# Kernel optimization log

Measured on AMD Instinct MI355X. Metric: run time of the kernel, lower is better.

## Reference

```python
import jax, jax.numpy as jnp
import numpy as np

B, N, P, E, H, D, F, L = 16, 500, 100, 128, 8, 16, 512, 6
CLIP = 10.0  # logit_clipping


def _heads(x, h):
    b, n, _ = x.shape
    return x.reshape(b, n, h, -1).transpose(0, 2, 1, 3)  # [b,h,n,d]


def _mha(q, k, v, mask3=None):
    d = q.shape[-1]
    s = jnp.einsum('bhnd,bhmd->bhnm', q, k) / jnp.sqrt(jnp.asarray(d, q.dtype))
    if mask3 is not None:
        s = s + mask3[:, None, :, :]
    w = jax.nn.softmax(s, axis=-1)
    o = jnp.einsum('bhnm,bhmd->bhnd', w, v)
    b, h, n, dd = o.shape
    return o.transpose(0, 2, 1, 3).reshape(b, n, h * dd)


def _ff(x, w1, b1, w2, b2):
    return jax.nn.relu(x @ w1 + b1) @ w2 + b2


def _forward(depot_xy, node_xy, node_demand, load, cur_dist, ninf_mask,
             emb_depot_w, emb_depot_b, emb_node_w, emb_node_b,
             enc_wq, enc_wk, enc_wv, enc_comb_w, enc_comb_b,
             enc_ff1_w, enc_ff1_b, enc_ff2_w, enc_ff2_b,
             dec_wq_last, dec_wk, dec_wv, dec_comb_w, dec_comb_b,
             dec_cap_w, dec_ff1_w, dec_ff1_b, dec_ff2_w, dec_ff2_b,
             current_node):
    # ---------------- encoder ----------------
    node_xy_demand = jnp.concatenate([node_xy, node_demand[:, :, None]], axis=2)  # [B,N,3]
    x = jnp.concatenate([depot_xy @ emb_depot_w + emb_depot_b,
                         node_xy_demand @ emb_node_w + emb_node_b], axis=1)  # [B,N+1,E]
    for i in range(L):
        q = _heads(x @ enc_wq[i], H)
        k = _heads(x @ enc_wk[i], H)
        v = _heads(x @ enc_wv[i], H)
        mh = _mha(q, k, v) @ enc_comb_w[i] + enc_comb_b[i]
        o1 = x + mh
        x = o1 + _ff(o1, enc_ff1_w[i], enc_ff1_b[i], enc_ff2_w[i], enc_ff2_b[i])
    encoded_nodes = x  # [B, N+1, E]
    # decoder kv cache (set_kv)
    k = _heads(encoded_nodes @ dec_wk, H)
    v = _heads(encoded_nodes @ dec_wv, H)
    # ---------------- one decode step ----------------
    encoded_last = jnp.take_along_axis(encoded_nodes, current_node[:, :, None], axis=1)  # [B,P,E]
    input_cat = jnp.concatenate([encoded_last, load[:, :, None]], axis=2)  # [B,P,E+1]
    q = _heads(input_cat @ dec_wq_last, H)
    mh = _mha(q, k, v, mask3=ninf_mask) @ dec_comb_w + dec_comb_b
    mh = mh + encoded_last + load[:, :, None] @ dec_cap_w
    q_ref = _ff(mh, dec_ff1_w, dec_ff1_b, dec_ff2_w, dec_ff2_b) + mh
    score = jnp.einsum('bpe,bne->bpn', q_ref, encoded_nodes) / jnp.sqrt(jnp.asarray(E, q_ref.dtype))
    # distance-based noise injection
    dmin = cur_dist.min(axis=-1, keepdims=True)
    dmax = cur_dist.max(axis=-1, keepdims=True)
    norm_dist = (cur_dist - dmin) / (dmax - dmin + 1e-6)
    problem_size = ninf_mask.shape[2]
    nm = 50.0 / problem_size
    base_noise = jax.random.normal(jax.random.key(42), cur_dist.shape, cur_dist.dtype) * 0.2 + 0.5
    score = score - (1.0 - nm) * jnp.log(norm_dist + 1e-6) + base_noise * nm
    score = CLIP * jnp.tanh(score) + ninf_mask
    return jax.nn.softmax(score, axis=2)  # [B,P,N+1]


def setup_inputs() -> dict:
    key = jax.random.key(0)
    ks = iter(jax.random.split(key, 40))
    def rn(shape, s=0.02):
        return s * jax.random.normal(next(ks), shape, jnp.float32)
    return dict(
        depot_xy=jax.random.uniform(next(ks), (B, 1, 2), jnp.float32),
        node_xy=jax.random.uniform(next(ks), (B, N, 2), jnp.float32),
        node_demand=jax.random.uniform(next(ks), (B, N), jnp.float32),
        load=jax.random.uniform(next(ks), (B, P), jnp.float32),
        cur_dist=jax.random.uniform(next(ks), (B, P, N + 1), jnp.float32),
        ninf_mask=jnp.zeros((B, P, N + 1), jnp.float32),
        current_node=jax.random.randint(next(ks), (B, P), 0, N + 1),
        emb_depot_w=rn((2, E)), emb_depot_b=rn((E,)),
        emb_node_w=rn((3, E)), emb_node_b=rn((E,)),
        enc_wq=rn((L, E, H * D)), enc_wk=rn((L, E, H * D)), enc_wv=rn((L, E, H * D)),
        enc_comb_w=rn((L, H * D, E)), enc_comb_b=rn((L, E)),
        enc_ff1_w=rn((L, E, F)), enc_ff1_b=rn((L, F)),
        enc_ff2_w=rn((L, F, E)), enc_ff2_b=rn((L, E)),
        dec_wq_last=rn((E + 1, H * D)), dec_wk=rn((E, H * D)), dec_wv=rn((E, H * D)),
        dec_comb_w=rn((H * D, E)), dec_comb_b=rn((E,)),
        dec_cap_w=rn((1, E)),
        dec_ff1_w=rn((E, F)), dec_ff1_b=rn((F,)),
        dec_ff2_w=rn((F, E)), dec_ff2_b=rn((E,)),
    )


def reference(depot_xy, node_xy, node_demand, load, cur_dist, ninf_mask, current_node,
              emb_depot_w, emb_depot_b, emb_node_w, emb_node_b,
              enc_wq, enc_wk, enc_wv, enc_comb_w, enc_comb_b,
              enc_ff1_w, enc_ff1_b, enc_ff2_w, enc_ff2_b,
              dec_wq_last, dec_wk, dec_wv, dec_comb_w, dec_comb_b,
              dec_cap_w, dec_ff1_w, dec_ff1_b, dec_ff2_w, dec_ff2_b):
    return _forward(depot_xy, node_xy, node_demand, load, cur_dist, ninf_mask,
                    emb_depot_w, emb_depot_b, emb_node_w, emb_node_b,
                    enc_wq, enc_wk, enc_wv, enc_comb_w, enc_comb_b,
                    enc_ff1_w, enc_ff1_b, enc_ff2_w, enc_ff2_b,
                    dec_wq_last, dec_wk, dec_wv, dec_comb_w, dec_comb_b,
                    dec_cap_w, dec_ff1_w, dec_ff1_b, dec_ff2_w, dec_ff2_b,
                    current_node)
```

## Files before the change

### kernel.cpp

```cpp
#include <hip/hip_runtime.h>
#include <math.h>

#define Bb 16
#define Nn 500
#define NT 501
#define Pp 100
#define Ee 128
#define Hh 8
#define Dd 16
#define Ff 512
#define Ll 6
#define Mtok (Bb*NT)
#define PR (Bb*Pp)
#define TJ 32
#define SPLIT 4
#define KSEG 126
#define DSPLIT 16
#define DSEG 32
#define ENCP (6*128*384)
#define DECP (128*256)
#define SNP 512

__global__ __launch_bounds__(256) void pack_k(
    const float* __restrict__ ewq, const float* __restrict__ ewk, const float* __restrict__ ewv,
    const float* __restrict__ dwk, const float* __restrict__ dwv,
    float* __restrict__ encP, float* __restrict__ decP)
{
  int i = blockIdx.x*256 + threadIdx.x;
  if (i < ENCP) {
    int l = i / (128*384); int rem = i - l*128*384; int k = rem / 384; int n = rem - k*384;
    float v;
    if (n < 128)      v = ewq[((size_t)l*128 + k)*128 + n];
    else if (n < 256) v = ewk[((size_t)l*128 + k)*128 + (n-128)];
    else              v = ewv[((size_t)l*128 + k)*128 + (n-256)];
    encP[i] = v;
  } else {
    int j = i - ENCP;
    if (j < DECP) {
      int k = j >> 8; int n = j & 255;
      decP[j] = (n < 128) ? dwk[k*128 + n] : dwv[k*128 + (n-128)];
    }
  }
}

__global__ __launch_bounds__(256) void embed_k(
    const float* __restrict__ depot_xy, const float* __restrict__ node_xy,
    const float* __restrict__ node_demand,
    const float* __restrict__ wD, const float* __restrict__ bD,
    const float* __restrict__ wN, const float* __restrict__ bN,
    float* __restrict__ x)
{
  int t = blockIdx.x*256 + threadIdx.x;
  if (t >= Mtok*Ee) return;
  int e   = t & (Ee-1);
  int tok = t >> 7;
  int b   = tok / NT;
  int n   = tok - b*NT;
  float v;
  if (n == 0) {
    v = depot_xy[b*2+0]*wD[0*Ee+e] + depot_xy[b*2+1]*wD[1*Ee+e] + bD[e];
  } else {
    int nn = n - 1;
    float c0 = node_xy[(b*Nn + nn)*2 + 0];
    float c1 = node_xy[(b*Nn + nn)*2 + 1];
    float c2 = node_demand[b*Nn + nn];
    v = c0*wN[0*Ee+e] + c1*wN[1*Ee+e] + c2*wN[2*Ee+e] + bN[e];
  }
  x[(size_t)tok*Ee + e] = v;
}

__global__ __launch_bounds__(256) void gemm_k(
    const float* __restrict__ A, const float* __restrict__ W,
    const float* __restrict__ bias, const float* __restrict__ res,
    float* __restrict__ C, int M, int N, int K, int relu)
{
  __shared__ __align__(16) float As[2][16][68];
  __shared__ __align__(16) float Bs[2][16][68];
  int tid = threadIdx.x;
  int tx = tid & 15, ty = tid >> 4;
  int m0 = blockIdx.x * 64, n0 = blockIdx.y * 64;
  float acc[4][4];
  #pragma unroll
  for (int i=0;i<4;i++)
    #pragma unroll
    for (int j=0;j<4;j++) acc[i][j] = 0.f;

  int ar = tid >> 2;
  int ak = (tid & 3) << 2;
  int br = tid >> 4;
  int bc = (tid & 15) << 2;

  const float* Ap = A + (size_t)(m0 + ar)*K + ak;
  const float* Wp = W + (size_t)br*N + n0 + bc;
  bool aok = (m0 + ar) < M;

  float4 av = aok ? *(const float4*)(Ap) : make_float4(0.f,0.f,0.f,0.f);
  float4 wv = *(const float4*)(Wp);

  int nk = K >> 4;
  for (int t = 0; t < nk; ++t) {
    int cur = t & 1;
    As[cur][ak+0][ar] = av.x; As[cur][ak+1][ar] = av.y;
    As[cur][ak+2][ar] = av.z; As[cur][ak+3][ar] = av.w;
    *(float4*)(&Bs[cur][br][bc]) = wv;
    __syncthreads();
    if (t+1 < nk) {
      av = aok ? *(const float4*)(Ap + (t+1)*16) : make_float4(0.f,0.f,0.f,0.f);
      wv = *(const float4*)(Wp + (size_t)(t+1)*16*N);
    }
    #pragma unroll
    for (int k=0;k<16;k++){
      float4 a4 = *(const float4*)(&As[cur][k][ty*4]);
      float4 b4 = *(const float4*)(&Bs[cur][k][tx*4]);
      float avv[4] = {a4.x,a4.y,a4.z,a4.w};
      float bvv[4] = {b4.x,b4.y,b4.z,b4.w};
      #pragma unroll
      for (int i=0;i<4;i++)
        #pragma unroll
        for (int j=0;j<4;j++)
          acc[i][j] = fmaf(avv[i], bvv[j], acc[i][j]);
    }
  }

  float4 bv = make_float4(0.f,0.f,0.f,0.f);
  if (bias) bv = *(const float4*)(bias + n0 + tx*4);
  #pragma unroll
  for (int i=0;i<4;i++){
    int row = m0 + ty*4 + i;
    if (row >= M) continue;
    float4 o;
    o.x = acc[i][0] + bv.x; o.y = acc[i][1] + bv.y;
    o.z = acc[i][2] + bv.z; o.w = acc[i][3] + bv.w;
    if (relu){ o.x=fmaxf(o.x,0.f); o.y=fmaxf(o.y,0.f); o.z=fmaxf(o.z,0.f); o.w=fmaxf(o.w,0.f); }
    if (res){
      float4 rv = *(const float4*)(res + (size_t)row*N + n0 + tx*4);
      o.x += rv.x; o.y += rv.y; o.z += rv.z; o.w += rv.w;
    }
    *(float4*)(C + (size_t)row*N + n0 + tx*4) = o;
  }
}

__device__ __forceinline__ float dot4(float4 a, float4 b){
  return fmaf(a.x,b.x, fmaf(a.y,b.y, fmaf(a.z,b.z, a.w*b.w)));
}

__global__ __launch_bounds__(256, 1) void attn_enc_k(
    const float* __restrict__ QKV, float* __restrict__ part_o,
    float* __restrict__ part_l)
{
  int blk = blockIdx.x;
  int s  = blk % SPLIT;
  int bh = blk / SPLIT;
  int h  = bh & (Hh-1);
  int b  = bh >> 3;
  int tid = threadIdx.x;
  int p0 = tid;
  int p1 = tid + 256;
  const int klo = s*KSEG;
  int kseg = NT - klo; if (kseg > KSEG) kseg = KSEG;

  __shared__ __align__(16) float4 Ks[2][TJ][4];
  __shared__ __align__(16) float4 Vs[2][TJ][4];

  int row = (tid >> 2) & 31;
  int lc  = tid & 3;
  bool isV = tid >= 128;
  const int kvoff = isV ? 256 : 128;

  bool vbq = p1 < NT;

  const float4* qp0 = (const float4*)(QKV + ((size_t)(b*NT + p0))*384 + h*Dd);
  float4 qa0=qp0[0], qa1=qp0[1], qa2=qp0[2], qa3=qp0[3];
  float4 qb0,qb1,qb2,qb3;
  if (vbq) {
    const float4* qp1 = (const float4*)(QKV + ((size_t)(b*NT + p1))*384 + h*Dd);
    qb0=qp1[0]; qb1=qp1[1]; qb2=qp1[2]; qb3=qp1[3];
  } else {
    qb0=qb1=qb2=qb3=make_float4(0,0,0,0);
  }

  if (row < kseg) {
    float4 v = *((const float4*)(QKV + ((size_t)(b*NT + klo + row))*384 + kvoff + h*Dd) + lc);
    if (isV) Vs[0][row][lc] = v; else Ks[0][row][lc] = v;
  }
  __syncthreads();

  float lA = 0.f, lB = 0.f;
  float4 oA0=make_float4(0,0,0,0), oA1=oA0, oA2=oA0, oA3=oA0;
  float4 oB0=oA0, oB1=oA0, oB2=oA0, oB3=oA0;
  const int ntiles = (kseg + TJ - 1)/TJ;
  int buf = 0;

  for (int t = 0; t < ntiles; ++t) {
    int j0 = t*TJ;
    if (t+1 < ntiles) {
      int jj = j0 + TJ + row;
      if (jj < kseg) {
        float4 v = *((const float4*)(QKV + ((size_t)(b*NT + klo + jj))*384 + kvoff + h*Dd) + lc);
        if (isV) Vs[buf^1][row][lc] = v; else Ks[buf^1][row][lc] = v;
      }
    }
    int jend = kseg - j0; if (jend > TJ) jend = TJ;

    #pragma unroll 2
    for (int jj = 0; jj < jend; ++jj) {
      float4 k0=Ks[buf][jj][0], k1=Ks[buf][jj][1], k2=Ks[buf][jj][2], k3=Ks[buf][jj][3];
      float sA = (dot4(qa0,k0)+dot4(qa1,k1)) + (dot4(qa2,k2)+dot4(qa3,k3));
      float sB = (dot4(qb0,k0)+dot4(qb1,k1)) + (dot4(qb2,k2)+dot4(qb3,k3));
      float wA = __expf(sA*0.25f);
      float wB = __expf(sB*0.25f);
      lA += wA; lB += wB;
      float4 v0=Vs[buf][jj][0], v1=Vs[buf][jj][1], v2=Vs[buf][jj][2], v3=Vs[buf][jj][3];
      oA0.x=fmaf(wA,v0.x,oA0.x); oA0.y=fmaf(wA,v0.y,oA0.y); oA0.z=fmaf(wA,v0.z,oA0.z); oA0.w=fmaf(wA,v0.w,oA0.w);
      oA1.x=fmaf(wA,v1.x,oA1.x); oA1.y=fmaf(wA,v1.y,oA1.y); oA1.z=fmaf(wA,v1.z,oA1.z); oA1.w=fmaf(wA,v1.w,oA1.w);
      oA2.x=fmaf(wA,v2.x,oA2.x); oA2.y=fmaf(wA,v2.y,oA2.y); oA2.z=fmaf(wA,v2.z,oA2.z); oA2.w=fmaf(wA,v2.w,oA2.w);
      oA3.x=fmaf(wA,v3.x,oA3.x); oA3.y=fmaf(wA,v3.y,oA3.y); oA3.z=fmaf(wA,v3.z,oA3.z); oA3.w=fmaf(wA,v3.w,oA3.w);
      oB0.x=fmaf(wB,v0.x,oB0.x); oB0.y=fmaf(wB,v0.y,oB0.y); oB0.z=fmaf(wB,v0.z,oB0.z); oB0.w=fmaf(wB,v0.w,oB0.w);
      oB1.x=fmaf(wB,v1.x,oB1.x); oB1.y=fmaf(wB,v1.y,oB1.y); oB1.z=fmaf(wB,v1.z,oB1.z); oB1.w=fmaf(wB,v1.w,oB1.w);
      oB2.x=fmaf(wB,v2.x,oB2.x); oB2.y=fmaf(wB,v2.y,oB2.y); oB2.z=fmaf(wB,v2.z,oB2.z); oB2.w=fmaf(wB,v2.w,oB2.w);
      oB3.x=fmaf(wB,v3.x,oB3.x); oB3.y=fmaf(wB,v3.y,oB3.y); oB3.z=fmaf(wB,v3.z,oB3.z); oB3.w=fmaf(wB,v3.w,oB3.w);
    }
    __syncthreads();
    buf ^= 1;
  }

  size_t r0 = ((size_t)s*128 + bh)*NT + p0;
  float4* po0 = (float4*)(part_o + r0*16);
  po0[0]=oA0; po0[1]=oA1; po0[2]=oA2; po0[3]=oA3;
  part_l[r0] = lA;
  if (vbq) {
    size_t r1 = ((size_t)s*128 + bh)*NT + p1;
    float4* po1 = (float4*)(part_o + r1*16);
    po1[0]=oB0; po1[1]=oB1; po1[2]=oB2; po1[3]=oB3;
    part_l[r1] = lB;
  }
}

__global__ __launch_bounds__(256) void comb_gemm_k(
    const float* __restrict__ part_o, const float* __restrict__ part_l,
    const float* __restrict__ W, const float* __restrict__ bias,
    const float* __restrict__ res, float* __restrict__ C)
{
  __shared__ __align__(16) float As[2][16][68];
  __shared__ __align__(16) float Bs[2][16][68];
  int tid = threadIdx.x;
  int tx = tid & 15, ty = tid >> 4;
  int m0 = blockIdx.x * 64, n0 = blockIdx.y * 64;
  float acc[4][4];
  #pragma unroll
  for (int i=0;i<4;i++)
    #pragma unroll
    for (int j=0;j<4;j++) acc[i][j] = 0.f;

  int ar = tid >> 2;
  int ak = (tid & 3) << 2;
  int br = tid >> 4;
  int bc = (tid & 15) << 2;

  int row = m0 + ar;
  bool aok = row < Mtok;
  int tok = aok ? row : 0;
  int bb = tok / NT;
  int p  = tok - bb*NT;
  const size_t pbase = ((size_t)(bb*8))*NT + p;

  const float* Wp = W + (size_t)br*Ee + n0 + bc;

  #define LOADA(t, dst) { \
    float4 o4 = make_float4(0.f,0.f,0.f,0.f); float l = 0.f; \
    _Pragma("unroll") \
    for (int s=0;s<SPLIT;s++){ \
      size_t idx = (size_t)s*((size_t)128*NT) + pbase + (size_t)(t)*NT; \
      float4 v = *(const float4*)(part_o + idx*16 + ak); \
      o4.x+=v.x; o4.y+=v.y; o4.z+=v.z; o4.w+=v.w; \
      l += part_l[idx]; \
    } \
    float inv = aok ? 1.f/l : 0.f; \
    dst = make_float4(o4.x*inv, o4.y*inv, o4.z*inv, o4.w*inv); \
  }

  float4 av; LOADA(0, av);
  float4 wv = *(const float4*)(Wp);

  for (int t = 0; t < 8; ++t) {
    int cur = t & 1;
    As[cur][ak+0][ar] = av.x; As[cur][ak+1][ar] = av.y;
    As[cur][ak+2][ar] = av.z; As[cur][ak+3][ar] = av.w;
    *(float4*)(&Bs[cur][br][bc]) = wv;
    __syncthreads();
    if (t+1 < 8) {
      LOADA(t+1, av);
      wv = *(const float4*)(Wp + (size_t)(t+1)*16*Ee);
    }
    #pragma unroll
    for (int k=0;k<16;k++){
      float4 a4 = *(const float4*)(&As[cur][k][ty*4]);
      float4 b4 = *(const float4*)(&Bs[cur][k][tx*4]);
      float avv[4] = {a4.x,a4.y,a4.z,a4.w};
      float bvv[4] = {b4.x,b4.y,b4.z,b4.w};
      #pragma unroll
      for (int i=0;i<4;i++)
        #pragma unroll
        for (int j=0;j<4;j++)
          acc[i][j] = fmaf(avv[i], bvv[j], acc[i][j]);
    }
  }
  #undef LOADA

  float4 bv = *(const float4*)(bias + n0 + tx*4);
  #pragma unroll
  for (int i=0;i<4;i++){
    int orow = m0 + ty*4 + i;
    if (orow >= Mtok) continue;
    float4 o;
    float4 rv = *(const float4*)(res + (size_t)orow*Ee + n0 + tx*4);
    o.x = acc[i][0] + bv.x + rv.x; o.y = acc[i][1] + bv.y + rv.y;
    o.z = acc[i][2] + bv.z + rv.z; o.w = acc[i][3] + bv.w + rv.w;
    *(float4*)(C + (size_t)orow*Ee + n0 + tx*4) = o;
  }
}

__global__ __launch_bounds__(128) void attn_dec_k(
    const float* __restrict__ Q, const float* __restrict__ KV,
    const float* __restrict__ mask,
    float* __restrict__ part_o, float* __restrict__ part_l)
{
  int blk = blockIdx.x;
  int s  = blk & (DSPLIT-1);
  int bh = blk >> 4;
  int h  = bh & (Hh-1);
  int b  = bh >> 3;
  int klo = s*DSEG;
  int kn  = NT - klo; if (kn > DSEG) kn = DSEG;

  __shared__ __align__(16) float4 Ks[DSEG][4];
  __shared__ __align__(16) float4 Vs[DSEG][4];

  int tid = threadIdx.x;
  for (int i = tid; i < kn*8; i += 128) {
    int row  = i >> 3;
    int q8   = i & 7;
    int quad = q8 & 3;
    int isv  = q8 >> 2;
    float4 v = *(const float4*)(KV + ((size_t)(b*NT + klo + row))*256 + isv*128 + h*Dd + quad*4);
    if (isv) Vs[row][quad] = v; else Ks[row][quad] = v;
  }
  __syncthreads();

  int p = tid;
  if (p >= Pp) return;
  int r = b*Pp + p;
  const float4* qp = (const float4*)(Q + (size_t)r*Ee + h*Dd);
  float4 qa=qp[0], qb=qp[1], qc=qp[2], qd=qp[3];
  const float* mrow = mask + (size_t)r*NT + klo;

  float l = 0.f;
  float4 o0=make_float4(0,0,0,0), o1=o0, o2=o0, o3=o0;
  for (int j=0;j<kn;++j){
    float sc = (dot4(qa,Ks[j][0])+dot4(qb,Ks[j][1])) + (dot4(qc,Ks[j][2])+dot4(qd,Ks[j][3]));
    float w = __expf(sc*0.25f + mrow[j]);
    l += w;
    float4 v0=Vs[j][0],v1=Vs[j][1],v2=Vs[j][2],v3=Vs[j][3];
    o0.x=fmaf(w,v0.x,o0.x); o0.y=fmaf(w,v0.y,o0.y); o0.z=fmaf(w,v0.z,o0.z); o0.w=fmaf(w,v0.w,o0.w);
    o1.x=fmaf(w,v1.x,o1.x); o1.y=fmaf(w,v1.y,o1.y); o1.z=fmaf(w,v1.z,o1.z); o1.w=fmaf(w,v1.w,o1.w);
    o2.x=fmaf(w,v2.x,o2.x); o2.y=fmaf(w,v2.y,o2.y); o2.z=fmaf(w,v2.z,o2.z); o2.w=fmaf(w,v2.w,o2.w);
    o3.x=fmaf(w,v3.x,o3.x); o3.y=fmaf(w,v3.y,o3.y); o3.z=fmaf(w,v3.z,o3.z); o3.w=fmaf(w,v3.w,o3.w);
  }

  size_t rb = ((size_t)s*PR + r)*Hh + h;
  float4* po = (float4*)(part_o + rb*16);
  po[0]=o0; po[1]=o1; po[2]=o2; po[3]=o3;
  part_l[rb] = l;
}

__global__ __launch_bounds__(128) void decq_k(
    const float* __restrict__ x, const int* __restrict__ cur,
    const float* __restrict__ loadv, const float* __restrict__ Wq,
    float* __restrict__ q, float* __restrict__ encl)
{
  __shared__ float row[Ee];
  int r = blockIdx.x, e = threadIdx.x;
  int b = r / Pp;
  int node = cur[r];
  float xv = x[((size_t)(b*NT + node))*Ee + e];
  encl[(size_t)r*Ee + e] = xv;
  row[e] = xv;
  __syncthreads();
  float acc = 0.f;
  #pragma unroll 4
  for (int k=0;k<Ee;k++) acc = fmaf(row[k], Wq[k*128 + e], acc);
  acc = fmaf(loadv[r], Wq[Ee*128 + e], acc);
  q[(size_t)r*128 + e] = acc;
}

__global__ __launch_bounds__(128) void dec_comb_k(
    const float* __restrict__ dpart_o, const float* __restrict__ dpart_l,
    const float* __restrict__ W, const float* __restrict__ bias,
    const float* __restrict__ encl, const float* __restrict__ loadv,
    const float* __restrict__ capw, float* __restrict__ mh)
{
  __shared__ float row[Ee];
  int r = blockIdx.x, e = threadIdx.x;
  int h = e >> 4, d = e & 15;
  const size_t S = (size_t)PR*Hh;
  size_t rb = (size_t)r*Hh + h;
  float L = 0.f, o = 0.f;
  #pragma unroll
  for (int s=0;s<DSPLIT;s++){
    L += dpart_l[(size_t)s*S + rb];
    o += dpart_o[((size_t)s*S + rb)*16 + d];
  }
  row[e] = o / L;
  __syncthreads();
  float acc = 0.f;
  #pragma unroll 4
  for (int k=0;k<Ee;k++) acc = fmaf(row[k], W[k*Ee + e], acc);
  mh[(size_t)r*Ee + e] = acc + bias[e] + encl[(size_t)r*Ee + e] + loadv[r]*capw[e];
}

__global__ __launch_bounds__(256) void xt_k(
    const float* __restrict__ x, float* __restrict__ xT)
{
  __shared__ float T[32][33];
  int n0 = blockIdx.x * 32;
  int k0 = blockIdx.y * 32;
  int b  = blockIdx.z;
  int t  = threadIdx.x;
  int row = t >> 3;
  int c4  = (t & 7) << 2;

  int n = n0 + row;
  float4 v = make_float4(0.f,0.f,0.f,0.f);
  if (n < NT) v = *(const float4*)(x + ((size_t)(b*NT + n))*Ee + k0 + c4);
  T[c4+0][row] = v.x; T[c4+1][row] = v.y; T[c4+2][row] = v.z; T[c4+3][row] = v.w;
  __syncthreads();

  const float SC = 0.08838834764831845f;
  float4 o;
  o.x = T[row][c4+0]*SC; o.y = T[row][c4+1]*SC;
  o.z = T[row][c4+2]*SC; o.w = T[row][c4+3]*SC;
  *(float4*)(xT + ((size_t)(b*Ee + k0 + row))*SNP + n0 + c4) = o;
}

__global__ __launch_bounds__(256) void score_gemm_k(
    const float* __restrict__ qref, const float* __restrict__ xT,
    float* __restrict__ score)
{
  __shared__ __align__(16) float As[2][16][68];
  __shared__ __align__(16) float Bs[2][16][68];
  int tid = threadIdx.x;
  int tx = tid & 15, ty = tid >> 4;
  int m0 = blockIdx.x * 64;
  int n0 = blockIdx.y * 64;
  int b  = blockIdx.z;

  const float* A = qref + (size_t)b*Pp*Ee;
  const float* W = xT   + (size_t)b*Ee*SNP;
  float*       C = score + (size_t)b*Pp*SNP;

  float acc[4][4];
  #pragma unroll
  for (int i=0;i<4;i++)
    #pragma unroll
    for (int j=0;j<4;j++) acc[i][j] = 0.f;

  int ar = tid >> 2;
  int ak = (tid & 3) << 2;
  int br = tid >> 4;
  int bc = (tid & 15) << 2;

  const float* Ap = A + (size_t)(m0 + ar)*Ee + ak;
  const float* Wp = W + (size_t)br*SNP + n0 + bc;
  bool aok = (m0 + ar) < Pp;

  float4 av = aok ? *(const float4*)(Ap) : make_float4(0.f,0.f,0.f,0.f);
  float4 wv = *(const float4*)(Wp);

  for (int t = 0; t < 8; ++t) {
    int cur = t & 1;
    As[cur][ak+0][ar] = av.x; As[cur][ak+1][ar] = av.y;
    As[cur][ak+2][ar] = av.z; As[cur][ak+3][ar] = av.w;
    *(float4*)(&Bs[cur][br][bc]) = wv;
    __syncthreads();
    if (t+1 < 8) {
      av = aok ? *(const float4*)(Ap + (t+1)*16) : make_float4(0.f,0.f,0.f,0.f);
      wv = *(const float4*)(Wp + (size_t)(t+1)*16*SNP);
    }
    #pragma unroll
    for (int k=0;k<16;k++){
      float4 a4 = *(const float4*)(&As[cur][k][ty*4]);
      float4 b4 = *(const float4*)(&Bs[cur][k][tx*4]);
      float avv[4] = {a4.x,a4.y,a4.z,a4.w};
      float bvv[4] = {b4.x,b4.y,b4.z,b4.w};
      #pragma unroll
      for (int i=0;i<4;i++)
        #pragma unroll
        for (int j=0;j<4;j++)
          acc[i][j] = fmaf(avv[i], bvv[j], acc[i][j]);
    }
    __syncthreads();
  }

  #pragma unroll
  for (int i=0;i<4;i++){
    int row = m0 + ty*4 + i;
    if (row >= Pp) continue;
    float4 o;
    o.x = acc[i][0]; o.y = acc[i][1]; o.z = acc[i][2]; o.w = acc[i][3];
    *(float4*)(C + (size_t)row*SNP + n0 + tx*4) = o;
  }
}

__device__ __forceinline__ unsigned rotl32(unsigned x, int r){ return (x<<r)|(x>>(32-r)); }

__device__ float tf_normal(unsigned idx)
{
  unsigned x0 = 0u;
  unsigned x1 = idx;
  const unsigned ks[3] = {0u, 42u, 0u ^ 42u ^ 0x1BD11BDAu};
  x0 += ks[0]; x1 += ks[1];
  const int rotA[4] = {13,15,26,6};
  const int rotB[4] = {17,29,16,24};
  #pragma unroll
  for (int i=0;i<5;i++){
    #pragma unroll
    for (int q=0;q<4;q++){
      int rr = (i&1) ? rotB[q] : rotA[q];
      x0 += x1; x1 = rotl32(x1, rr); x1 ^= x0;
    }
    x0 += ks[(i+1)%3];
    x1 += ks[(i+2)%3] + (unsigned)(i+1);
  }
  unsigned bits = x0 ^ x1;
  float f = __uint_as_float((bits >> 9) | 0x3f800000u) - 1.0f;
  const float lo = -0.99999994f;
  float u = f * 2.0f + lo;
  u = fmaxf(lo, u);
  float w = -log1pf(-u*u);
  float p;
  if (w < 5.0f) {
    w -= 2.5f;
    p = 2.81022636e-08f;
    p = fmaf(p, w, 3.43273939e-07f);
    p = fmaf(p, w, -3.5233877e-06f);
    p = fmaf(p, w, -4.39150654e-06f);
    p = fmaf(p, w, 0.00021858087f);
    p = fmaf(p, w, -0.00125372503f);
    p = fmaf(p, w, -0.00417768164f);
    p = fmaf(p, w, 0.246640727f);
    p = fmaf(p, w, 1.50140941f);
  } else {
    w = sqrtf(w) - 3.0f;
    p = -0.000200214257f;
    p = fmaf(p, w, 0.000100950558f);
    p = fmaf(p, w, 0.00134934322f);
    p = fmaf(p, w, -0.00367342844f);
    p = fmaf(p, w, 0.00573950773f);
    p = fmaf(p, w, -0.0076224613f);
    p = fmaf(p, w, 0.00943887047f);
    p = fmaf(p, w, 1.00167406f);
    p = fmaf(p, w, 2.83297682f);
  }
  return 1.4142135623730951f * (p * u);
}

__global__ __launch_bounds__(512) void final_k(
    const float* __restrict__ score, const float* __restrict__ cur_dist,
    const float* __restrict__ ninf, float* __restrict__ out)
{
  __shared__ float smn[8], smx[8], sm2[8], ss[8];
  const float NM = (float)(50.0/501.0);
  const float C1 = (float)(1.0 - 50.0/501.0);
  int r = blockIdx.x;
  int t = threadIdx.x;
  int wid = t >> 6, lane = t & 63;

  float cd = 0.f;
  float mn = 1e30f, mx = -1e30f;
  if (t < NT) { cd = cur_dist[(size_t)r*NT + t]; mn = cd; mx = cd; }
  #pragma unroll
  for (int off=32; off>=1; off>>=1){
    mn = fminf(mn, __shfl_xor(mn, off));
    mx = fmaxf(mx, __shfl_xor(mx, off));
  }
  if (lane == 0){ smn[wid] = mn; smx[wid] = mx; }
  __syncthreads();
  float dmin = smn[0], dmax = smx[0];
  #pragma unroll
  for (int i=1;i<8;i++){ dmin = fminf(dmin, smn[i]); dmax = fmaxf(dmax, smx[i]); }

  float sval = -1e30f;
  if (t < NT) {
    float nd = (cd - dmin) / (dmax - dmin + 1e-6f);
    float z  = tf_normal((unsigned)r*501u + (unsigned)t);
    float s  = score[(size_t)r*SNP + t] - C1*logf(nd + 1e-6f) + (z*0.2f + 0.5f)*NM;
    sval = 10.0f*tanhf(s) + ninf[(size_t)r*NT + t];
  }
  float mv = sval;
  #pragma unroll
  for (int off=32; off>=1; off>>=1) mv = fmaxf(mv, __shfl_xor(mv, off));
  if (lane == 0) sm2[wid] = mv;
  __syncthreads();
  float smax = sm2[0];
  #pragma unroll
  for (int i=1;i<8;i++) smax = fmaxf(smax, sm2[i]);

  float e = (t < NT) ? expf(sval - smax) : 0.f;
  float sv = e;
  #pragma unroll
  for (int off=32; off>=1; off>>=1) sv += __shfl_xor(sv, off);
  if (lane == 0) ss[wid] = sv;
  __syncthreads();
  float ssum = ss[0];
  #pragma unroll
  for (int i=1;i<8;i++) ssum += ss[i];

  if (t < NT) out[(size_t)r*NT + t] = e / ssum;
}

extern "C" void kernel_launch(void* const* d_in, const int* in_sizes, int n_in,
                              void* d_out, int out_size, void* d_ws, size_t ws_size,
                              hipStream_t stream)
{
  (void)in_sizes; (void)n_in; (void)out_size; (void)ws_size;
  const float* depot_xy    = (const float*)d_in[0];
  const float* node_xy     = (const float*)d_in[1];
  const float* node_demand = (const float*)d_in[2];
  const float* loadv       = (const float*)d_in[3];
  const float* cur_dist    = (const float*)d_in[4];
  const float* ninf        = (const float*)d_in[5];
  const int*   cur_node    = (const int*)d_in[6];
  const float* emb_depot_w = (const float*)d_in[7];
  const float* emb_depot_b = (const float*)d_in[8];
  const float* emb_node_w  = (const float*)d_in[9];
  const float* emb_node_b  = (const float*)d_in[10];
  const float* enc_wq      = (const float*)d_in[11];
  const float* enc_wk      = (const float*)d_in[12];
  const float* enc_wv      = (const float*)d_in[13];
  const float* enc_comb_w  = (const float*)d_in[14];
  const float* enc_comb_b  = (const float*)d_in[15];
  const float* enc_ff1_w   = (const float*)d_in[16];
  const float* enc_ff1_b   = (const float*)d_in[17];
  const float* enc_ff2_w   = (const float*)d_in[18];
  const float* enc_ff2_b   = (const float*)d_in[19];
  const float* dec_wq_last = (const float*)d_in[20];
  const float* dec_wk      = (const float*)d_in[21];
  const float* dec_wv      = (const float*)d_in[22];
  const float* dec_comb_w  = (const float*)d_in[23];
  const float* dec_comb_b  = (const float*)d_in[24];
  const float* dec_cap_w   = (const float*)d_in[25];
  const float* dec_ff1_w   = (const float*)d_in[26];
  const float* dec_ff1_b   = (const float*)d_in[27];
  const float* dec_ff2_w   = (const float*)d_in[28];
  const float* dec_ff2_b   = (const float*)d_in[29];

  float* ws = (float*)d_ws;
  const size_t SZ = (size_t)Mtok*Ee;
  float* xb    = ws + 0*SZ;
  float* qkvb  = ws + 1*SZ;
  float* atb   = ws + 4*SZ;
  float* o1b   = ws + 5*SZ;
  float* ffb   = ws + 6*SZ;
  float* encPk = ws + 10*SZ;
  float* decPk = encPk + ENCP;
  float* part_o  = ffb;
  float* epart_l = atb;
  float* dpart_o = ffb;
  float* dpart_l = o1b;
  float* encl  = qkvb + 2*SZ;
  float* qdec  = encl + 204800;
  float* mhb   = qdec + 204800;
  float* qrefb = atb;
  float* ffh2  = ffb;
  float* xTb   = ffb;
  float* scoreb= o1b;

  pack_k<<<(ENCP + DECP + 255)/256, 256, 0, stream>>>(
      enc_wq, enc_wk, enc_wv, dec_wk, dec_wv, encPk, decPk);

  embed_k<<<(Mtok*Ee + 255)/256, 256, 0, stream>>>(
      depot_xy, node_xy, node_demand, emb_depot_w, emb_depot_b,
      emb_node_w, emb_node_b, xb);

  dim3 gqkv((Mtok + 63)/64, 384/64);
  dim3 gcombg((Mtok + 63)/64, Ee/64);
  dim3 gff ((Mtok + 63)/64, Ff/64);
  dim3 g128((Mtok + 63)/64, Ee/64);
  for (int l = 0; l < Ll; ++l) {
    gemm_k<<<gqkv, 256, 0, stream>>>(xb, encPk + (size_t)l*128*384, nullptr, nullptr, qkvb, Mtok, 384, Ee, 0);
    attn_enc_k<<<Bb*Hh*SPLIT, 256, 0, stream>>>(qkvb, part_o, epart_l);
    comb_gemm_k<<<gcombg, 256, 0, stream>>>(part_o, epart_l, enc_comb_w + (size_t)l*Ee*Ee,
                                            enc_comb_b + l*Ee, xb, o1b);
    gemm_k<<<gff, 256, 0, stream>>>(o1b, enc_ff1_w + (size_t)l*Ee*Ff, enc_ff1_b + l*Ff, nullptr, ffb, Mtok, Ff, Ee, 1);
    gemm_k<<<g128, 256, 0, stream>>>(ffb, enc_ff2_w + (size_t)l*Ff*Ee, enc_ff2_b + l*Ee, o1b, xb, Mtok, Ee, Ff, 0);
  }

  dim3 gkv((Mtok + 63)/64, 256/64);
  gemm_k<<<gkv, 256, 0, stream>>>(xb, decPk, nullptr, nullptr, qkvb, Mtok, 256, Ee, 0);
  decq_k<<<PR, 128, 0, stream>>>(xb, cur_node, loadv, dec_wq_last, qdec, encl);
  attn_dec_k<<<Bb*Hh*DSPLIT, 128, 0, stream>>>(qdec, qkvb, ninf, dpart_o, dpart_l);
  dec_comb_k<<<PR, 128, 0, stream>>>(dpart_o, dpart_l, dec_comb_w, dec_comb_b, encl, loadv, dec_cap_w, mhb);
  dim3 gd1((PR + 63)/64, Ff/64);
  gemm_k<<<gd1, 256, 0, stream>>>(mhb, dec_ff1_w, dec_ff1_b, nullptr, ffh2, PR, Ff, Ee, 1);
  dim3 gd2((PR + 63)/64, Ee/64);
  gemm_k<<<gd2, 256, 0, stream>>>(ffh2, dec_ff2_w, dec_ff2_b, mhb, qrefb, PR, Ee, Ff, 0);
  dim3 gxt(16, 4, 16);
  xt_k<<<gxt, 256, 0, stream>>>(xb, xTb);
  dim3 gsc(2, 8, 16);
  score_gemm_k<<<gsc, 256, 0, stream>>>(qrefb, xTb, scoreb);
  final_k<<<PR, 512, 0, stream>>>(scoreb, cur_dist, ninf, (float*)d_out);
}
```

Measured before the change: 936.3 us.

## Use split-bf16 MFMA (3-pass) in the generic GEMM instead of scalar FP32 FMAs

Rewrites the generic GEMM kernel to split each fp32 operand into high and low bf16 parts. It accumulates hi*hi + hi*lo + lo*hi with 16x16x32 bf16 MFMA instructions, tiling 64x64 per block with four waves each owning a 16-row strip. The aim is to move the encoder and decoder projection and FFN matmuls off scalar FMA units onto matrix cores while keeping near-fp32 accuracy. The costs are extra conversion work and scalar transposed shared-memory stores for W, and epilogue stores that are now scalar rather than float4.

New measurement: 980.5 us. +4.7%, slower.

```diff
diff --git a/kernel.cpp b/kernel.cpp
--- a/kernel.cpp
+++ b/kernel.cpp
@@ -20,6 +20,22 @@
 #define ENCP (6*128*384)
 #define DECP (128*256)
 #define SNP 512
+#define KP 36
+
+typedef __attribute__((ext_vector_type(8))) short bf16x8;
+typedef __attribute__((ext_vector_type(4))) float f32x4;
+
+__device__ __forceinline__ unsigned short bfhi(float x){
+  union { float f; unsigned u; } c; c.f = x; return (unsigned short)(c.u >> 16);
+}
+__device__ __forceinline__ float bff(unsigned short h){
+  union { float f; unsigned u; } c; c.u = ((unsigned)h) << 16; return c.f;
+}
+__device__ __forceinline__ uint2 pack4(unsigned short a, unsigned short b,
+                                       unsigned short c, unsigned short d){
+  uint2 r; r.x = (unsigned)a | ((unsigned)b << 16);
+  r.y = (unsigned)c | ((unsigned)d << 16); return r;
+}
 
 __global__ __launch_bounds__(256) void pack_k(
     const float* __restrict__ ewq, const float* __restrict__ ewk, const float* __restrict__ ewv,
@@ -74,70 +90,111 @@
     const float* __restrict__ bias, const float* __restrict__ res,
     float* __restrict__ C, int M, int N, int K, int relu)
 {
-  __shared__ __align__(16) float As[2][16][68];
-  __shared__ __align__(16) float Bs[2][16][68];
+  __shared__ __align__(16) unsigned short Ah[2][64][KP];
+  __shared__ __align__(16) unsigned short Al[2][64][KP];
+  __shared__ __align__(16) unsigned short Bh[2][64][KP];
+  __shared__ __align__(16) unsigned short Bl[2][64][KP];
+
   int tid = threadIdx.x;
-  int tx = tid & 15, ty = tid >> 4;
   int m0 = blockIdx.x * 64, n0 = blockIdx.y * 64;
-  float acc[4][4];
-  #pragma unroll
-  for (int i=0;i<4;i++)
-    #pragma unroll
-    for (int j=0;j<4;j++) acc[i][j] = 0.f;
+  int wvid = tid >> 6;
+  int lane = tid & 63;
+  int lrow = lane & 15;
+  int lk8  = (lane >> 4) * 8;
+
+  f32x4 acc0 = {0.f,0.f,0.f,0.f}, acc1 = acc0, acc2 = acc0, acc3 = acc0;
 
   int ar = tid >> 2;
-  int ak = (tid & 3) << 2;
-  int br = tid >> 4;
-  int bc = (tid & 15) << 2;
-
-  const float* Ap = A + (size_t)(m0 + ar)*K + ak;
-  const float* Wp = W + (size_t)br*N + n0 + bc;
+  int ac = (tid & 3) << 2;
+  int wr = tid >> 4;
+  int wc = (tid & 15) << 2;
+
+  const float* Ap = A + (size_t)(m0 + ar)*K + ac;
+  const float* Wp = W + (size_t)wr*N + n0 + wc;
   bool aok = (m0 + ar) < M;
 
-  float4 av = aok ? *(const float4*)(Ap) : make_float4(0.f,0.f,0.f,0.f);
-  float4 wv = *(const float4*)(Wp);
-
-  int nk = K >> 4;
+  float4 zz = make_float4(0.f,0.f,0.f,0.f);
+  float4 av0 = aok ? *(const float4*)(Ap)      : zz;
+  float4 av1 = aok ? *(const float4*)(Ap + 16) : zz;
+  float4 wv0 = *(const float4*)(Wp);
+  float4 wv1 = *(const float4*)(Wp + (size_t)16*N);
+
+  int nk = K >> 5;
   for (int t = 0; t < nk; ++t) {
     int cur = t & 1;
-    As[cur][ak+0][ar] = av.x; As[cur][ak+1][ar] = av.y;
-    As[cur][ak+2][ar] = av.z; As[cur][ak+3][ar] = av.w;
-    *(float4*)(&Bs[cur][br][bc]) = wv;
+    {
+      unsigned short h0=bfhi(av0.x), h1=bfhi(av0.y), h2=bfhi(av0.z), h3=bfhi(av0.w);
+      unsigned short l0=bfhi(av0.x-bff(h0)), l1=bfhi(av0.y-bff(h1)),
+                     l2=bfhi(av0.z-bff(h2)), l3=bfhi(av0.w-bff(h3));
+      *(uint2*)&Ah[cur][ar][ac] = pack4(h0,h1,h2,h3);
+      *(uint2*)&Al[cur][ar][ac] = pack4(l0,l1,l2,l3);
+      h0=bfhi(av1.x); h1=bfhi(av1.y); h2=bfhi(av1.z); h3=bfhi(av1.w);
+      l0=bfhi(av1.x-bff(h0)); l1=bfhi(av1.y-bff(h1));
+      l2=bfhi(av1.z-bff(h2)); l3=bfhi(av1.w-bff(h3));
+      *(uint2*)&Ah[cur][ar][ac+16] = pack4(h0,h1,h2,h3);
+      *(uint2*)&Al[cur][ar][ac+16] = pack4(l0,l1,l2,l3);
+    }
+    {
+      float w4[4] = {wv0.x, wv0.y, wv0.z, wv0.w};
+      #pragma unroll
+      for (int i=0;i<4;i++){
+        unsigned short h = bfhi(w4[i]);
+        Bh[cur][wc+i][wr] = h;
+        Bl[cur][wc+i][wr] = bfhi(w4[i] - bff(h));
+      }
+      float w5[4] = {wv1.x, wv1.y, wv1.z, wv1.w};
+      #pragma unroll
+      for (int i=0;i<4;i++){
+        unsigned short h = bfhi(w5[i]);
+        Bh[cur][wc+i][wr+16] = h;
+        Bl[cur][wc+i][wr+16] = bfhi(w5[i] - bff(h));
+      }
+    }
     __syncthreads();
     if (t+1 < nk) {
-      av = aok ? *(const float4*)(Ap + (t+1)*16) : make_float4(0.f,0.f,0.f,0.f);
-      wv = *(const float4*)(Wp + (size_t)(t+1)*16*N);
-    }
-    #pragma unroll
-    for (int k=0;k<16;k++){
-      float4 a4 = *(const float4*)(&As[cur][k][ty*4]);
-      float4 b4 = *(const float4*)(&Bs[cur][k][tx*4]);
-      float avv[4] = {a4.x,a4.y,a4.z,a4.w};
-      float bvv[4] = {b4.x,b4.y,b4.z,b4.w};
-      #pragma unroll
-      for (int i=0;i<4;i++)
-        #pragma unroll
-        for (int j=0;j<4;j++)
-          acc[i][j] = fmaf(avv[i], bvv[j], acc[i][j]);
-    }
-  }
-
-  float4 bv = make_float4(0.f,0.f,0.f,0.f);
-  if (bias) bv = *(const float4*)(bias + n0 + tx*4);
-  #pragma unroll
-  for (int i=0;i<4;i++){
-    int row = m0 + ty*4 + i;
-    if (row >= M) continue;
-    float4 o;
-    o.x = acc[i][0] + bv.x; o.y = acc[i][1] + bv.y;
-    o.z = acc[i][2] + bv.z; o.w = acc[i][3] + bv.w;
-    if (relu){ o.x=fmaxf(o.x,0.f); o.y=fmaxf(o.y,0.f); o.z=fmaxf(o.z,0.f); o.w=fmaxf(o.w,0.f); }
-    if (res){
-      float4 rv = *(const float4*)(res + (size_t)row*N + n0 + tx*4);
-      o.x += rv.x; o.y += rv.y; o.z += rv.z; o.w += rv.w;
-    }
-    *(float4*)(C + (size_t)row*N + n0 + tx*4) = o;
-  }
+      av0 = aok ? *(const float4*)(Ap + (size_t)(t+1)*32)      : zz;
+      av1 = aok ? *(const float4*)(Ap + (size_t)(t+1)*32 + 16) : zz;
+      wv0 = *(const float4*)(Wp + (size_t)(t+1)*32*N);
+      wv1 = *(const float4*)(Wp + ((size_t)(t+1)*32 + 16)*N);
+    }
+    union FR { bf16x8 v; uint2 u[2]; };
+    FR ah, al;
+    ah.u[0] = *(const uint2*)&Ah[cur][wvid*16 + lrow][lk8];
+    ah.u[1] = *(const uint2*)&Ah[cur][wvid*16 + lrow][lk8+4];
+    al.u[0] = *(const uint2*)&Al[cur][wvid*16 + lrow][lk8];
+    al.u[1] = *(const uint2*)&Al[cur][wvid*16 + lrow][lk8+4];
+    #define DOFRAG(f, accv) { \
+      FR bh, bl; \
+      bh.u[0] = *(const uint2*)&Bh[cur][(f)*16 + lrow][lk8]; \
+      bh.u[1] = *(const uint2*)&Bh[cur][(f)*16 + lrow][lk8+4]; \
+      bl.u[0] = *(const uint2*)&Bl[cur][(f)*16 + lrow][lk8]; \
+      bl.u[1] = *(const uint2*)&Bl[cur][(f)*16 + lrow][lk8+4]; \
+      accv = __builtin_amdgcn_mfma_f32_16x16x32_bf16(ah.v, bh.v, accv, 0,0,0); \
+      accv = __builtin_amdgcn_mfma_f32_16x16x32_bf16(ah.v, bl.v, accv, 0,0,0); \
+      accv = __builtin_amdgcn_mfma_f32_16x16x32_bf16(al.v, bh.v, accv, 0,0,0); \
+    }
+    DOFRAG(0, acc0); DOFRAG(1, acc1); DOFRAG(2, acc2); DOFRAG(3, acc3);
+    #undef DOFRAG
+  }
+
+  int crow0 = m0 + wvid*16 + (lane >> 4)*4;
+  int col0  = n0 + lrow;
+  #define WRFRAG(f, accv) { \
+    int col = col0 + (f)*16; \
+    float bvs = bias ? bias[col] : 0.f; \
+    _Pragma("unroll") \
+    for (int j=0;j<4;j++){ \
+      int row = crow0 + j; \
+      if (row < M) { \
+        float v = accv[j] + bvs; \
+        if (relu) v = fmaxf(v, 0.f); \
+        if (res) v += res[(size_t)row*N + col]; \
+        C[(size_t)row*N + col] = v; \
+      } \
+    } \
+  }
+  WRFRAG(0, acc0); WRFRAG(1, acc1); WRFRAG(2, acc2); WRFRAG(3, acc3);
+  #undef WRFRAG
 }
 
 __device__ __forceinline__ float dot4(float4 a, float4 b){
```
